# Kernel optimization log

Measured on AMD Instinct MI355X. Metric: run time of the kernel, lower is better.

Reference implementation:

```python
import jax, jax.numpy as jnp
import numpy as np

N_QUBITS = 4
Q_DEPTH = 6
Q_DELTA = 0.01
BATCH = 65536


def _apply_ry(state, theta, q):
    """Apply RY(theta) on qubit q. state: [B,2,2,2,2]; theta: [B] (per-sample) or scalar.
    RY = [[cos(t/2), -sin(t/2)], [sin(t/2), cos(t/2)]] (PennyLane convention, real)."""
    c = jnp.cos(theta * 0.5)
    s = jnp.sin(theta * 0.5)
    s0 = jnp.take(state, 0, axis=q + 1)  # [B,2,2,2]
    s1 = jnp.take(state, 1, axis=q + 1)
    if jnp.ndim(theta) == 1:  # per-sample angle -> broadcast over remaining qubit axes
        c = c[:, None, None, None]
        s = s[:, None, None, None]
    new0 = c * s0 - s * s1
    new1 = s * s0 + c * s1
    return jnp.stack([new0, new1], axis=q + 1)


def _cnot(state, ctrl, tgt):
    """CNOT with control `ctrl`, target `tgt` on state [B,2,2,2,2]."""
    s0 = jnp.take(state, 0, axis=ctrl + 1)
    s1 = jnp.take(state, 1, axis=ctrl + 1)
    # target axis index inside the reduced (rank-4) array
    t_ax = tgt + 1 if tgt < ctrl else tgt
    s1 = jnp.flip(s1, axis=t_ax)
    return jnp.stack([s0, s1], axis=ctrl + 1)


def quantum_circuit(q_in, q_params):
    """Batched 4-qubit variational circuit. q_in: [B,4], q_params: [24].
    Circuit is real-valued (H, RY, CNOT on |0...0>), so state is float."""
    B = q_in.shape[0]
    # H layer on |0000> -> uniform amplitude 1/4 over all 16 basis states
    state = jnp.full((B, 2, 2, 2, 2), 0.25, dtype=q_in.dtype)
    for q in range(N_QUBITS):
        state = _apply_ry(state, q_in[:, q], q)
    qw = q_params.reshape(Q_DEPTH, N_QUBITS)
    for k in range(Q_DEPTH):
        # entangling layer: CNOT(0,1), CNOT(2,3), then CNOT(1,2)
        state = _cnot(state, 0, 1)
        state = _cnot(state, 2, 3)
        state = _cnot(state, 1, 2)
        for q in range(N_QUBITS):
            state = _apply_ry(state, qw[k, q], q)
    probs = state * state  # [B,2,2,2,2]
    zs = []
    for q in range(N_QUBITS):
        other = tuple(a for a in (1, 2, 3, 4) if a != q + 1)
        m = probs.sum(axis=other)  # [B,2]
        zs.append(m[:, 0] - m[:, 1])  # <Z_q> = P(0) - P(1)
    return jnp.stack(zs, axis=1)  # [B,4]


def setup_inputs() -> dict:
    key = jax.random.key(0)
    k1, k2, k3, k4 = jax.random.split(key, 4)
    return {
        "input_features": jax.random.normal(k1, (BATCH, 512), dtype=jnp.float32),
        "W_pre": jax.random.normal(k2, (N_QUBITS, 512), dtype=jnp.float32) * (1.0 / np.sqrt(512.0)),
        "b_pre": jnp.zeros((N_QUBITS,), dtype=jnp.float32),
        "q_params": Q_DELTA * jax.random.normal(k3, (Q_DEPTH * N_QUBITS,), dtype=jnp.float32),
        "W_post": jax.random.normal(k4, (200, N_QUBITS), dtype=jnp.float32) * 0.5,
        "b_post": jnp.zeros((200,), dtype=jnp.float32),
    }


def reference(input_features, W_pre, b_pre, q_params, W_post, b_post):
    pre_out = input_features @ W_pre.T + b_pre          # [B,4]
    q_in = jnp.tanh(pre_out) * (np.pi / 2.0)            # scale to (-pi/2, pi/2)
    q_out = quantum_circuit(q_in, q_params)             # [B,4]
    return q_out @ W_post.T + b_post                    # [B,200]
```

## Files before the change

kernel.cpp:

```cpp
#include <hip/hip_runtime.h>


#define BLOCK 256
#define WS 16
#define SPB 64

typedef float f4 __attribute__((ext_vector_type(4)));

__device__ __forceinline__ f4 ntload4(const float* p) {
  return __builtin_nontemporal_load((const f4*)p);
}

__device__ __forceinline__ float rs_step(float v0, float v1, bool hi, int m) {
  const float sd = hi ? v0 : v1;
  const float kp = hi ? v1 : v0;
  return kp + __shfl_xor(sd, m, 64);
}

template<int Q>
__device__ __forceinline__ void apply_ry(float (&st)[16], float c, float s) {
  constexpr int pos = 3 - Q;
  #pragma unroll
  for (int i = 0; i < 16; ++i) {
    if (((i >> pos) & 1) == 0) {
      const int j = i | (1 << pos);
      const float a = st[i], b = st[j];
      st[i] = c * a - s * b;
      st[j] = s * a + c * b;
    }
  }
}

template<int C, int T>
__device__ __forceinline__ void cnot(float (&st)[16]) {
  constexpr int pc = 3 - C, pt = 3 - T;
  #pragma unroll
  for (int i = 0; i < 16; ++i) {
    if ((((i >> pc) & 1) == 1) && (((i >> pt) & 1) == 0)) {
      const int j = i | (1 << pt);
      const float t = st[i]; st[i] = st[j]; st[j] = t;
    }
  }
}

__global__ __launch_bounds__(BLOCK, 4) void dqnet_kernel(
    const float* __restrict__ in, const float* __restrict__ Wpre,
    const float* __restrict__ bpre, const float* __restrict__ qp,
    const float* __restrict__ Wpost, const float* __restrict__ bpost,
    float* __restrict__ out) {
  __shared__ float s_wpost[200 * 4];
  __shared__ float s_bpost[200];
  __shared__ float s_c[24], s_sn[24];
  __shared__ f4 s_qout[SPB];

  const int tid = threadIdx.x;
  const int lane = tid & 63;
  const int wave = tid >> 6;

  if (tid < 200) {
    ((f4*)s_wpost)[tid] = ((const f4*)Wpost)[tid];
    s_bpost[tid] = bpost[tid];
  } else if (tid < 224) {
    const int k = tid - 200;
    const float a = qp[k] * 0.5f;
    s_c[k] = __cosf(a);
    s_sn[k] = __sinf(a);
  }

  f4 wa[4], wb[4];
  #pragma unroll
  for (int q = 0; q < 4; ++q) {
    wa[q] = *(const f4*)(Wpre + q * 512 + lane * 4);
    wb[q] = *(const f4*)(Wpre + q * 512 + 256 + lane * 4);
  }

  const int tile = blockIdx.x * SPB + wave * WS;
  const float* rb = in + (size_t)tile * 512 + lane * 4;

  const bool b1 = (lane & 1) != 0;
  const bool b2 = (lane & 2) != 0;

  float part[WS];
  f4 pxa[2], pxb[2];
  pxa[0] = ntload4(rb);        pxb[0] = ntload4(rb + 256);
  pxa[1] = ntload4(rb + 512);  pxb[1] = ntload4(rb + 512 + 256);
  #pragma unroll
  for (int s = 0; s < WS; ++s) {
    const f4 xa = pxa[s & 1], xb = pxb[s & 1];
    if (s + 2 < WS) {
      pxa[s & 1] = ntload4(rb + (size_t)(s + 2) * 512);
      pxb[s & 1] = ntload4(rb + (size_t)(s + 2) * 512 + 256);
    }
    float p0 = xa.x*wa[0].x + xa.y*wa[0].y + xa.z*wa[0].z + xa.w*wa[0].w
             + xb.x*wb[0].x + xb.y*wb[0].y + xb.z*wb[0].z + xb.w*wb[0].w;
    float p1 = xa.x*wa[1].x + xa.y*wa[1].y + xa.z*wa[1].z + xa.w*wa[1].w
             + xb.x*wb[1].x + xb.y*wb[1].y + xb.z*wb[1].z + xb.w*wb[1].w;
    float p2 = xa.x*wa[2].x + xa.y*wa[2].y + xa.z*wa[2].z + xa.w*wa[2].w
             + xb.x*wb[2].x + xb.y*wb[2].y + xb.z*wb[2].z + xb.w*wb[2].w;
    float p3 = xa.x*wa[3].x + xa.y*wa[3].y + xa.z*wa[3].z + xa.w*wa[3].w
             + xb.x*wb[3].x + xb.y*wb[3].y + xb.z*wb[3].z + xb.w*wb[3].w;
    const float a01 = rs_step(p0, p1, b1, 1);
    const float a23 = rs_step(p2, p3, b1, 1);
    part[s] = rs_step(a01, a23, b2, 2);
  }

  const bool b4  = (lane & 4)  != 0;
  const bool b8  = (lane & 8)  != 0;
  const bool b16 = (lane & 16) != 0;
  const bool b32 = (lane & 32) != 0;
  float a8[8], a4[4], a2[2];
  #pragma unroll
  for (int u = 0; u < 8; ++u) a8[u] = rs_step(part[2*u], part[2*u+1], b4, 4);
  #pragma unroll
  for (int u = 0; u < 4; ++u) a4[u] = rs_step(a8[2*u], a8[2*u+1], b8, 8);
  #pragma unroll
  for (int u = 0; u < 2; ++u) a2[u] = rs_step(a4[2*u], a4[2*u+1], b16, 16);
  const float r = rs_step(a2[0], a2[1], b32, 32);

  const float g0 = __shfl(r, (lane << 2) | 0, 64);
  const float g1 = __shfl(r, (lane << 2) | 1, 64);
  const float g2 = __shfl(r, (lane << 2) | 2, 64);
  const float g3 = __shfl(r, (lane << 2) | 3, 64);

  __syncthreads();

  if (lane < WS) {
    constexpr float PI_4 = 0.7853981633974483f;
    float st[16];
    #pragma unroll
    for (int i = 0; i < 16; ++i) st[i] = 0.25f;

    float sv, cv;
    __sincosf(tanhf(g0 + bpre[0]) * PI_4, &sv, &cv); apply_ry<0>(st, cv, sv);
    __sincosf(tanhf(g1 + bpre[1]) * PI_4, &sv, &cv); apply_ry<1>(st, cv, sv);
    __sincosf(tanhf(g2 + bpre[2]) * PI_4, &sv, &cv); apply_ry<2>(st, cv, sv);
    __sincosf(tanhf(g3 + bpre[3]) * PI_4, &sv, &cv); apply_ry<3>(st, cv, sv);

    #pragma unroll
    for (int k = 0; k < 6; ++k) {
      cnot<0,1>(st); cnot<2,3>(st); cnot<1,2>(st);
      apply_ry<0>(st, s_c[k*4+0], s_sn[k*4+0]);
      apply_ry<1>(st, s_c[k*4+1], s_sn[k*4+1]);
      apply_ry<2>(st, s_c[k*4+2], s_sn[k*4+2]);
      apply_ry<3>(st, s_c[k*4+3], s_sn[k*4+3]);
    }

    float p[16];
    #pragma unroll
    for (int i = 0; i < 16; ++i) p[i] = st[i] * st[i];
    float z0 = 0.f, z1 = 0.f, z2 = 0.f, z3 = 0.f;
    #pragma unroll
    for (int i = 0; i < 16; ++i) {
      z0 += ((i >> 3) & 1) ? -p[i] : p[i];
      z1 += ((i >> 2) & 1) ? -p[i] : p[i];
      z2 += ((i >> 1) & 1) ? -p[i] : p[i];
      z3 += ((i     ) & 1) ? -p[i] : p[i];
    }
    f4 z; z.x = z0; z.y = z1; z.z = z2; z.w = z3;
    s_qout[wave * WS + lane] = z;
  }
  __syncthreads();

  float* ob = out + (size_t)blockIdx.x * (SPB * 200);
  #pragma unroll
  for (int i = 0; i < 13; ++i) {
    const int idx4 = tid + i * BLOCK;
    if (idx4 < 3200) {
      const int sloc = idx4 / 50;
      const int j4 = idx4 - sloc * 50;
      const f4 qo = s_qout[sloc];
      const f4* wrow = (const f4*)&s_wpost[j4 * 16];
      const float* br = &s_bpost[j4 * 4];
      f4 o;
      o.x = br[0] + wrow[0].x*qo.x + wrow[0].y*qo.y + wrow[0].z*qo.z + wrow[0].w*qo.w;
      o.y = br[1] + wrow[1].x*qo.x + wrow[1].y*qo.y + wrow[1].z*qo.z + wrow[1].w*qo.w;
      o.z = br[2] + wrow[2].x*qo.x + wrow[2].y*qo.y + wrow[2].z*qo.z + wrow[2].w*qo.w;
      o.w = br[3] + wrow[3].x*qo.x + wrow[3].y*qo.y + wrow[3].z*qo.z + wrow[3].w*qo.w;
      __builtin_nontemporal_store(o, (f4*)(ob + (size_t)idx4 * 4));
    }
  }
}

extern "C" void kernel_launch(void* const* d_in, const int* in_sizes, int n_in,
                              void* d_out, int out_size, void* d_ws, size_t ws_size,
                              hipStream_t stream) {
  const float* in    = (const float*)d_in[0];
  const float* Wpre  = (const float*)d_in[1];
  const float* bpre  = (const float*)d_in[2];
  const float* qp    = (const float*)d_in[3];
  const float* Wpost = (const float*)d_in[4];
  const float* bpost = (const float*)d_in[5];
  float* out = (float*)d_out;

  const int B = in_sizes[0] / 512;
  const int nblk = B / SPB;
  dqnet_kernel<<<nblk, BLOCK, 0, stream>>>(in, Wpre, bpre, qp, Wpost, bpost, out);
}
```

Measured before the change: 205.4 us.

## Shrink per-block sample count, fast tanh, and product-state init for circuit

Reduces samples per wave from 16 to 4 (and per block from 64 to 16), launching four times as many blocks and shortening the shuffle-reduction tree, with the remaining lanes folded by xor shuffles. Replaces tanhf with an exp/rcp based approximation. Builds the initial state after the input RY layer directly as a tensor product of per-qubit amplitudes instead of applying four RY gates. More blocks raise parallelism and latency hiding, but each block repeats the W_post/b_post/cos-sin setup and has fewer loads in flight per wave.

```diff
diff --git a/kernel.cpp b/kernel.cpp
--- a/kernel.cpp
+++ b/kernel.cpp
@@ -2,13 +2,18 @@
 
 
 #define BLOCK 256
-#define WS 16
-#define SPB 64
+#define WS 4
+#define SPB 16
 
 typedef float f4 __attribute__((ext_vector_type(4)));
 
 __device__ __forceinline__ f4 ntload4(const float* p) {
   return __builtin_nontemporal_load((const f4*)p);
+}
+
+__device__ __forceinline__ float fast_tanh(float x) {
+  const float e = __expf(2.0f * x);
+  return 1.0f - 2.0f * __builtin_amdgcn_rcpf(e + 1.0f);
 }
 
 __device__ __forceinline__ float rs_step(float v0, float v1, bool hi, int m) {
@@ -104,18 +109,14 @@
     part[s] = rs_step(a01, a23, b2, 2);
   }
 
-  const bool b4  = (lane & 4)  != 0;
-  const bool b8  = (lane & 8)  != 0;
-  const bool b16 = (lane & 16) != 0;
-  const bool b32 = (lane & 32) != 0;
-  float a8[8], a4[4], a2[2];
-  #pragma unroll
-  for (int u = 0; u < 8; ++u) a8[u] = rs_step(part[2*u], part[2*u+1], b4, 4);
-  #pragma unroll
-  for (int u = 0; u < 4; ++u) a4[u] = rs_step(a8[2*u], a8[2*u+1], b8, 8);
-  #pragma unroll
-  for (int u = 0; u < 2; ++u) a2[u] = rs_step(a4[2*u], a4[2*u+1], b16, 16);
-  const float r = rs_step(a2[0], a2[1], b32, 32);
+  const bool b4 = (lane & 4) != 0;
+  const bool b8 = (lane & 8) != 0;
+  float a2[2];
+  a2[0] = rs_step(part[0], part[1], b4, 4);
+  a2[1] = rs_step(part[2], part[3], b4, 4);
+  float r = rs_step(a2[0], a2[1], b8, 8);
+  r += __shfl_xor(r, 16, 64);
+  r += __shfl_xor(r, 32, 64);
 
   const float g0 = __shfl(r, (lane << 2) | 0, 64);
   const float g1 = __shfl(r, (lane << 2) | 1, 64);
@@ -126,15 +127,21 @@
 
   if (lane < WS) {
     constexpr float PI_4 = 0.7853981633974483f;
+    float c[4], sn[4], sv, cv;
+    __sincosf(fast_tanh(g0 + bpre[0]) * PI_4, &sv, &cv); c[0] = cv; sn[0] = sv;
+    __sincosf(fast_tanh(g1 + bpre[1]) * PI_4, &sv, &cv); c[1] = cv; sn[1] = sv;
+    __sincosf(fast_tanh(g2 + bpre[2]) * PI_4, &sv, &cv); c[2] = cv; sn[2] = sv;
+    __sincosf(fast_tanh(g3 + bpre[3]) * PI_4, &sv, &cv); c[3] = cv; sn[3] = sv;
+
+    const float u0 = (c[0] - sn[0]) * 0.25f, v0 = (c[0] + sn[0]) * 0.25f;
+    const float u1 =  c[1] - sn[1],          v1 =  c[1] + sn[1];
+    const float u2 =  c[2] - sn[2],          v2 =  c[2] + sn[2];
+    const float u3 =  c[3] - sn[3],          v3 =  c[3] + sn[3];
+    const float thi[4] = {u0*u1, u0*v1, v0*u1, v0*v1};
+    const float tlo[4] = {u2*u3, u2*v3, v2*u3, v2*v3};
     float st[16];
     #pragma unroll
-    for (int i = 0; i < 16; ++i) st[i] = 0.25f;
-
-    float sv, cv;
-    __sincosf(tanhf(g0 + bpre[0]) * PI_4, &sv, &cv); apply_ry<0>(st, cv, sv);
-    __sincosf(tanhf(g1 + bpre[1]) * PI_4, &sv, &cv); apply_ry<1>(st, cv, sv);
-    __sincosf(tanhf(g2 + bpre[2]) * PI_4, &sv, &cv); apply_ry<2>(st, cv, sv);
-    __sincosf(tanhf(g3 + bpre[3]) * PI_4, &sv, &cv); apply_ry<3>(st, cv, sv);
+    for (int i = 0; i < 16; ++i) st[i] = thi[i >> 2] * tlo[i & 3];
 
     #pragma unroll
     for (int k = 0; k < 6; ++k) {
@@ -163,9 +170,9 @@
 
   float* ob = out + (size_t)blockIdx.x * (SPB * 200);
   #pragma unroll
-  for (int i = 0; i < 13; ++i) {
+  for (int i = 0; i < 4; ++i) {
     const int idx4 = tid + i * BLOCK;
-    if (idx4 < 3200) {
+    if (idx4 < SPB * 50) {
       const int sloc = idx4 / 50;
       const int j4 = idx4 - sloc * 50;
       const f4 qo = s_qout[sloc];
```

Result: no change. 207.6 us (+1.1%).
